# Kernel optimization log

Hardware: AMD Instinct MI355X
Metric: run time of the kernel (lower is better)

## Reference

```python
import jax, jax.numpy as jnp
import numpy as np

ERR = 1e-12


def setup_inputs() -> dict:
    key = jax.random.key(0)
    k1, k2, k3 = jax.random.split(key, 3)
    B, H, L, D = 2, 16, 2048, 64
    k = jax.random.normal(k1, (B, H, L, D), dtype=jnp.float32)
    src = jax.random.uniform(k2, (B, H, L), dtype=jnp.float32)
    dest = jax.random.uniform(k3, (B, H, L), dtype=jnp.float32)
    return {"k": k, "src": src, "dest": dest}


def reference(k, src, dest):
    # k: [B,H,L,D], src/dest: [B,H,L]
    L = k.shape[-2]
    s = jnp.sqrt(src + ERR)   # sqrt-scaled source weights
    d = jnp.sqrt(dest + ERR)  # sqrt-scaled destination weights
    # affinity_1[b,h,i,j] = s_i * d_j * (k_i . k_j), fused as (k*s) @ (k*d)^T
    a1 = jnp.einsum("bhid,bhjd->bhij", k * s[..., :, None], k * d[..., :, None])
    # relu then (x+err)^(2/3)  (kernel: exp2(log2(relu(a)+err) * 2/3))
    a3 = jnp.exp2(jnp.log2(jax.nn.relu(a1) + ERR) * (2.0 / 3.0))
    # forward cumulative sum over j, output causally masked to j >= i
    cs = jnp.cumsum(a3, axis=-1)
    idx = jnp.arange(L)
    mask = idx[:, None] <= idx[None, :]  # keep j >= i
    return jnp.where(mask, cs, 0.0)
```

## Files before the change

### kernel.cpp

```cpp
#include <hip/hip_runtime.h>

#define BH   32
#define LSEQ 2048
#define DDIM 64
#define ERRC 1e-12f

typedef __attribute__((ext_vector_type(8)))  short bf16x8;
typedef __attribute__((ext_vector_type(4)))  float floatx4;
typedef __attribute__((ext_vector_type(4)))  unsigned short ushort4v;

__device__ __forceinline__ unsigned short f2bf(float f) {
    unsigned u = __float_as_uint(f);
    u = u + 0x7FFFu + ((u >> 16) & 1u);
    return (unsigned short)(u >> 16);
}

__device__ __forceinline__ bf16x8 pack8s(const float* __restrict__ p, float w) {
    const floatx4* pv = (const floatx4*)p;
    floatx4 x = pv[0], y = pv[1];
    bf16x8 r;
    r[0] = (short)f2bf(x[0] * w); r[1] = (short)f2bf(x[1] * w);
    r[2] = (short)f2bf(x[2] * w); r[3] = (short)f2bf(x[3] * w);
    r[4] = (short)f2bf(y[0] * w); r[5] = (short)f2bf(y[1] * w);
    r[6] = (short)f2bf(y[2] * w); r[7] = (short)f2bf(y[3] * w);
    return r;
}

__global__ __launch_bounds__(256) void prep_kd(const float* __restrict__ k,
                                               const float* __restrict__ dest,
                                               unsigned short* __restrict__ kd) {
    int idx4 = blockIdx.x * 256 + threadIdx.x;
    int row  = idx4 >> 4;
    float d = sqrtf(dest[row] + ERRC);
    floatx4 v = ((const floatx4*)k)[idx4];
    ushort4v od;
#pragma unroll
    for (int r = 0; r < 4; ++r) od[r] = f2bf(v[r] * d);
    ((ushort4v*)kd)[idx4] = od;
}

__device__ __forceinline__ void load_frag(const unsigned short* __restrict__ p,
                                          bf16x8& lo, bf16x8& hi) {
    lo = *(const bf16x8*)p;
    hi = *(const bf16x8*)(p + 32);
}

__device__ __forceinline__ void load_b_raw(const float* __restrict__ k,
                                           const float* __restrict__ src,
                                           int bhL, int row, int q,
                                           bf16x8& lo, bf16x8& hi) {
    const float* p = k + (long)(bhL + row) * DDIM + q * 8;
    float s = sqrtf(src[bhL + row] + ERRC);
    lo = pack8s(p, s);
    hi = pack8s(p + 32, s);
}

__global__ __launch_bounds__(256, 4) void strip_sums(const unsigned short* __restrict__ kd,
                                                     const float* __restrict__ k,
                                                     const float* __restrict__ src,
                                                     float* __restrict__ S) {
    const int tid  = threadIdx.x;
    const int wave = tid >> 6;
    const int lane = tid & 63;
    const int q    = lane >> 4;
    const int l16  = lane & 15;
    const int bh   = blockIdx.x & 31;
    const int ib   = blockIdx.x >> 5;
    const int i0   = (ib * 4 + wave) * 16;
    const int bhL  = bh * LSEQ;
    const unsigned short* kdb = kd + (long)bh * LSEQ * DDIM;

    bf16x8 blo, bhi;
    load_b_raw(k, src, bhL, i0 + l16, q, blo, bhi);

    bf16x8 aLo[4], aHi[4];
#pragma unroll
    for (int t = 0; t < 4; ++t)
        load_frag(kdb + (long)(16 * t + l16) * DDIM + q * 8, aLo[t], aHi[t]);

    const float c23 = 2.0f / 3.0f;
    float ssv[3];

    for (int cc = 0; cc < 3; ++cc) {
        float ss = 0.f;
        for (int g = 0; g < 8; ++g) {
            const int jn = (cc * 8 + g < 23) ? (cc * 512 + g * 64 + 64) : 0;
            bf16x8 nLo[4], nHi[4];
#pragma unroll
            for (int t = 0; t < 4; ++t)
                load_frag(kdb + (long)(jn + 16 * t + l16) * DDIM + q * 8, nLo[t], nHi[t]);

            floatx4 acc[4];
#pragma unroll
            for (int t = 0; t < 4; ++t) {
                floatx4 z4 = {0.f, 0.f, 0.f, 0.f};
                z4 = __builtin_amdgcn_mfma_f32_16x16x32_bf16(aLo[t], blo, z4, 0, 0, 0);
                acc[t] = __builtin_amdgcn_mfma_f32_16x16x32_bf16(aHi[t], bhi, z4, 0, 0, 0);
            }

            float s = 0.f;
#pragma unroll
            for (int t = 0; t < 4; ++t)
#pragma unroll
                for (int r = 0; r < 4; ++r) {
                    float v = fmaxf(acc[t][r], 0.f) + ERRC;
                    s += exp2f(c23 * __log2f(v));
                }
            float s1 = s + __shfl_xor(s, 16, 64);
            ss += s1 + __shfl_xor(s1, 32, 64);

#pragma unroll
            for (int t = 0; t < 4; ++t) { aLo[t] = nLo[t]; aHi[t] = nHi[t]; }
        }
        ssv[cc] = ss;
    }

    float sv = (q == 0) ? ssv[0] : (q == 1) ? ssv[1] : ssv[2];
    if (q < 3)
        S[(long)(bhL + i0 + l16) * 4 + q] = sv;
}

__global__ __launch_bounds__(128, 4) void chunk_out2(const unsigned short* __restrict__ kd,
                                                     const float* __restrict__ k,
                                                     const float* __restrict__ src,
                                                     const float* __restrict__ S,
                                                     float* __restrict__ out) {
    const int tid  = threadIdx.x;
    const int wave = tid >> 6;
    const int lane = tid & 63;
    const int q    = lane >> 4;
    const int l16  = lane & 15;
    const int u    = blockIdx.x * 2 + wave;
    const int c    = u & 3;
    const int bh   = (u >> 2) & 31;
    const int it   = u >> 7;
    const int i0   = it << 4;
    const int bhL  = bh * LSEQ;
    const int jb   = c << 9;

    if (jb + 512 <= i0) {
        const floatx4 z = {0.f, 0.f, 0.f, 0.f};
#pragma unroll
        for (int s = 0; s < 16; ++s) {
            float* row = out + (long)(bhL + i0 + s) * LSEQ + jb + 4 * lane;
            *(floatx4*)row = z;
            *(floatx4*)(row + 256) = z;
        }
        return;
    }

    const unsigned short* kdb = kd + (long)bh * LSEQ * DDIM;

    bf16x8 blo, bhi;
    load_b_raw(k, src, bhL, i0 + l16, q, blo, bhi);

    float carry = 0.f;
    const float* Sr = S + (long)(bhL + i0 + l16) * 4;
#pragma unroll
    for (int cc = 0; cc < 3; ++cc)
        if (cc < c) carry += Sr[cc];

    const float c23 = 2.0f / 3.0f;

    bf16x8 aLo[4], aHi[4];
#pragma unroll
    for (int t = 0; t < 4; ++t)
        load_frag(kdb + (long)(jb + 16 * t + l16) * DDIM + q * 8, aLo[t], aHi[t]);

    float* orow = out + (long)(bhL + i0 + l16) * LSEQ + q * 4;

    for (int g = 0; g < 8; ++g) {
        const int j0 = jb + (g << 6);
        const int jn = jb + ((g < 7) ? ((g + 1) << 6) : 0);

        bf16x8 nLo[4], nHi[4];
#pragma unroll
        for (int t = 0; t < 4; ++t)
            load_frag(kdb + (long)(jn + 16 * t + l16) * DDIM + q * 8, nLo[t], nHi[t]);

        floatx4 acc[4];
#pragma unroll
        for (int t = 0; t < 4; ++t) {
            floatx4 z4 = {0.f, 0.f, 0.f, 0.f};
            z4 = __builtin_amdgcn_mfma_f32_16x16x32_bf16(aLo[t], blo, z4, 0, 0, 0);
            acc[t] = __builtin_amdgcn_mfma_f32_16x16x32_bf16(aHi[t], bhi, z4, 0, 0, 0);
        }

        float uu[4][4];
#pragma unroll
        for (int t = 0; t < 4; ++t)
#pragma unroll
            for (int r = 0; r < 4; ++r) {
                float v = fmaxf(acc[t][r], 0.f) + ERRC;
                uu[t][r] = exp2f(c23 * __log2f(v));
            }

        if (j0 + 64 <= i0) {
            float s = 0.f;
#pragma unroll
            for (int t = 0; t < 4; ++t)
                s += (uu[t][0] + uu[t][1]) + (uu[t][2] + uu[t][3]);
            float s1 = s + __shfl_xor(s, 16, 64);
            carry += s1 + __shfl_xor(s1, 32, 64);
            const floatx4 z = {0.f, 0.f, 0.f, 0.f};
#pragma unroll
            for (int t = 0; t < 4; ++t)
                *(floatx4*)(orow + j0 + 16 * t) = z;
        } else {
#pragma unroll
            for (int t = 0; t < 4; ++t) {
                const int jt0 = j0 + 16 * t;
                if (jt0 + 16 <= i0) {
                    float s = (uu[t][0] + uu[t][1]) + (uu[t][2] + uu[t][3]);
                    float s1 = s + __shfl_xor(s, 16, 64);
                    carry += s1 + __shfl_xor(s1, 32, 64);
                    const floatx4 z = {0.f, 0.f, 0.f, 0.f};
                    *(floatx4*)(orow + jt0) = z;
                } else {
                    uu[t][1] += uu[t][0];
                    uu[t][2] += uu[t][1];
                    uu[t][3] += uu[t][2];
                    const float Sg  = uu[t][3];
                    const float x16 = __shfl_xor(Sg, 16, 64);
                    const float s1  = Sg + x16;
                    const float x32 = __shfl_xor(s1, 32, 64);
                    const float E = ((q & 1) ? x16 : 0.f) + ((q & 2) ? x32 : 0.f) + carry;
                    carry += s1 + x32;
                    floatx4 o;
                    if (jt0 == i0) {
#pragma unroll
                        for (int r = 0; r < 4; ++r)
                            o[r] = ((q * 4 + r) >= l16) ? (uu[t][r] + E) : 0.f;
                    } else {
#pragma unroll
                        for (int r = 0; r < 4; ++r)
                            o[r] = uu[t][r] + E;
                    }
                    *(floatx4*)(orow + jt0) = o;
                }
            }
        }

#pragma unroll
        for (int t = 0; t < 4; ++t) { aLo[t] = nLo[t]; aHi[t] = nHi[t]; }
    }
}

__device__ __forceinline__ void load_row16_raw(const float* __restrict__ kp, long base, int row,
                                               int q, const float* __restrict__ w, int bhL,
                                               bf16x8& lo, bf16x8& hi) {
    const float* p = kp + base + (long)row * DDIM + q * 8;
    float s = sqrtf(w[bhL + row] + ERRC);
    lo = pack8s(p, s);
    hi = pack8s(p + 32, s);
}

__global__ __launch_bounds__(256, 4) void mha_raw(const float* __restrict__ kp,
                                                  const float* __restrict__ src,
                                                  const float* __restrict__ dest,
                                                  float* __restrict__ out) {
    const int tid  = threadIdx.x;
    const int wave = tid >> 6;
    const int lane = tid & 63;
    const int q    = lane >> 4;
    const int l16  = lane & 15;
    const int bh = blockIdx.x & 31;
    const int ib = blockIdx.x >> 5;
    const int i0 = (ib * 4 + wave) * 16;
    const int bhL = bh * LSEQ;
    const long base = (long)bh * LSEQ * DDIM;

    bf16x8 blo, bhi;
    load_row16_raw(kp, base, i0 + l16, q, src, bhL, blo, bhi);

    float carry = 0.f;
    const float c23 = 2.0f / 3.0f;

    bf16x8 aLo[4], aHi[4];
#pragma unroll
    for (int t = 0; t < 4; ++t)
        load_row16_raw(kp, base, 16 * t + l16, q, dest, bhL, aLo[t], aHi[t]);

    float* orow = out + (long)(bhL + i0 + l16) * LSEQ + q * 4;

    for (int it = 0; it < 32; ++it) {
        const int j0 = it << 6;
        bf16x8 nLo[4], nHi[4];
        const int jn = (it < 31) ? (j0 + 64) : 0;
#pragma unroll
        for (int t = 0; t < 4; ++t)
            load_row16_raw(kp, base, jn + 16 * t + l16, q, dest, bhL, nLo[t], nHi[t]);

        floatx4 acc[4];
#pragma unroll
        for (int t = 0; t < 4; ++t) {
            floatx4 z4 = {0.f, 0.f, 0.f, 0.f};
            z4 = __builtin_amdgcn_mfma_f32_16x16x32_bf16(aLo[t], blo, z4, 0, 0, 0);
            acc[t] = __builtin_amdgcn_mfma_f32_16x16x32_bf16(aHi[t], bhi, z4, 0, 0, 0);
        }

        float uu[4][4];
#pragma unroll
        for (int t = 0; t < 4; ++t)
#pragma unroll
            for (int r = 0; r < 4; ++r) {
                float v = fmaxf(acc[t][r], 0.f) + ERRC;
                uu[t][r] = exp2f(c23 * __log2f(v));
            }

#pragma unroll
        for (int t = 0; t < 4; ++t) {
            const int jt0 = j0 + 16 * t;
            if (jt0 + 16 <= i0) {
                float s = (uu[t][0] + uu[t][1]) + (uu[t][2] + uu[t][3]);
                float s1 = s + __shfl_xor(s, 16, 64);
                carry += s1 + __shfl_xor(s1, 32, 64);
                const floatx4 z = {0.f, 0.f, 0.f, 0.f};
                *(floatx4*)(orow + jt0) = z;
            } else {
                uu[t][1] += uu[t][0];
                uu[t][2] += uu[t][1];
                uu[t][3] += uu[t][2];
                const float Sg  = uu[t][3];
                const float x16 = __shfl_xor(Sg, 16, 64);
                const float s1  = Sg + x16;
                const float x32 = __shfl_xor(s1, 32, 64);
                const float E = ((q & 1) ? x16 : 0.f) + ((q & 2) ? x32 : 0.f) + carry;
                carry += s1 + x32;
                floatx4 o;
                if (jt0 == i0) {
#pragma unroll
                    for (int r = 0; r < 4; ++r)
                        o[r] = ((q * 4 + r) >= l16) ? (uu[t][r] + E) : 0.f;
                } else {
#pragma unroll
                    for (int r = 0; r < 4; ++r)
                        o[r] = uu[t][r] + E;
                }
                *(floatx4*)(orow + jt0) = o;
            }
        }

#pragma unroll
        for (int t = 0; t < 4; ++t) { aLo[t] = nLo[t]; aHi[t] = nHi[t]; }
    }
}

extern "C" void kernel_launch(void* const* d_in, const int* in_sizes, int n_in,
                              void* d_out, int out_size, void* d_ws, size_t ws_size,
                              hipStream_t stream) {
    const float* k    = (const float*)d_in[0];
    const float* src  = (const float*)d_in[1];
    const float* dest = (const float*)d_in[2];
    float* out = (float*)d_out;

    const size_t kdsz = (size_t)BH * LSEQ * DDIM * sizeof(unsigned short);
    const size_t ssz  = (size_t)BH * LSEQ * 4 * sizeof(float);
    if (ws_size >= kdsz + ssz) {
        unsigned short* kd = (unsigned short*)d_ws;
        float* S = (float*)((char*)d_ws + kdsz);
        prep_kd<<<dim3(4096), dim3(256), 0, stream>>>(k, dest, kd);
        strip_sums<<<dim3(1024), dim3(256), 0, stream>>>(kd, k, src, S);
        chunk_out2<<<dim3(8192), dim3(128), 0, stream>>>(kd, k, src, S, out);
    } else {
        mha_raw<<<dim3(1024), dim3(256), 0, stream>>>(k, src, dest, out);
    }
}
```

Baseline: 706.9 us.

## Split strip sums per chunk, drop register prefetch, remap waves for occupancy

The strip-sum kernel now gives each wave a single 512-column chunk, not all three chunks in sequence, so the grid grows threefold and work spreads across more waves. Both kernels drop the double-buffered next-fragment prefetch, which lowers register pressure. Launch bounds rise to 8 blocks per CU and the wave-to-work mapping becomes bh-fastest with 256-thread blocks. The cost is exposed load latency per tile and extra wave launches.

```diff
diff --git a/kernel.cpp b/kernel.cpp
--- a/kernel.cpp
+++ b/kernel.cpp
@@ -55,72 +55,57 @@
     hi = pack8s(p + 32, s);
 }
 
-__global__ __launch_bounds__(256, 4) void strip_sums(const unsigned short* __restrict__ kd,
-                                                     const float* __restrict__ k,
-                                                     const float* __restrict__ src,
-                                                     float* __restrict__ S) {
+__global__ __launch_bounds__(256, 8) void strip_sums2(const unsigned short* __restrict__ kd,
+                                                      const float* __restrict__ k,
+                                                      const float* __restrict__ src,
+                                                      float* __restrict__ S) {
     const int tid  = threadIdx.x;
     const int wave = tid >> 6;
     const int lane = tid & 63;
     const int q    = lane >> 4;
     const int l16  = lane & 15;
-    const int bh   = blockIdx.x & 31;
-    const int ib   = blockIdx.x >> 5;
-    const int i0   = (ib * 4 + wave) * 16;
+    const int u    = blockIdx.x * 4 + wave;
+    const int bh   = u & 31;
+    const int rest = u >> 5;
+    const int it   = rest & 127;
+    const int cc   = rest >> 7;
+    const int i0   = it << 4;
     const int bhL  = bh * LSEQ;
+    const int jb   = cc << 9;
     const unsigned short* kdb = kd + (long)bh * LSEQ * DDIM;
 
     bf16x8 blo, bhi;
     load_b_raw(k, src, bhL, i0 + l16, q, blo, bhi);
 
-    bf16x8 aLo[4], aHi[4];
-#pragma unroll
-    for (int t = 0; t < 4; ++t)
-        load_frag(kdb + (long)(16 * t + l16) * DDIM + q * 8, aLo[t], aHi[t]);
-
     const float c23 = 2.0f / 3.0f;
-    float ssv[3];
-
-    for (int cc = 0; cc < 3; ++cc) {
-        float ss = 0.f;
-        for (int g = 0; g < 8; ++g) {
-            const int jn = (cc * 8 + g < 23) ? (cc * 512 + g * 64 + 64) : 0;
-            bf16x8 nLo[4], nHi[4];
-#pragma unroll
-            for (int t = 0; t < 4; ++t)
-                load_frag(kdb + (long)(jn + 16 * t + l16) * DDIM + q * 8, nLo[t], nHi[t]);
-
-            floatx4 acc[4];
-#pragma unroll
-            for (int t = 0; t < 4; ++t) {
-                floatx4 z4 = {0.f, 0.f, 0.f, 0.f};
-                z4 = __builtin_amdgcn_mfma_f32_16x16x32_bf16(aLo[t], blo, z4, 0, 0, 0);
-                acc[t] = __builtin_amdgcn_mfma_f32_16x16x32_bf16(aHi[t], bhi, z4, 0, 0, 0);
-            }
-
-            float s = 0.f;
-#pragma unroll
-            for (int t = 0; t < 4; ++t)
-#pragma unroll
-                for (int r = 0; r < 4; ++r) {
-                    float v = fmaxf(acc[t][r], 0.f) + ERRC;
-                    s += exp2f(c23 * __log2f(v));
-                }
-            float s1 = s + __shfl_xor(s, 16, 64);
-            ss += s1 + __shfl_xor(s1, 32, 64);
-
-#pragma unroll
-            for (int t = 0; t < 4; ++t) { aLo[t] = nLo[t]; aHi[t] = nHi[t]; }
-        }
-        ssv[cc] = ss;
-    }
-
-    float sv = (q == 0) ? ssv[0] : (q == 1) ? ssv[1] : ssv[2];
-    if (q < 3)
-        S[(long)(bhL + i0 + l16) * 4 + q] = sv;
-}
-
-__global__ __launch_bounds__(128, 4) void chunk_out2(const unsigned short* __restrict__ kd,
+    float ss = 0.f;
+
+    for (int g = 0; g < 8; ++g) {
+        const int j0 = jb + (g << 6);
+        bf16x8 aLo[4], aHi[4];
+#pragma unroll
+        for (int t = 0; t < 4; ++t)
+            load_frag(kdb + (long)(j0 + 16 * t + l16) * DDIM + q * 8, aLo[t], aHi[t]);
+
+#pragma unroll
+        for (int t = 0; t < 4; ++t) {
+            floatx4 z4 = {0.f, 0.f, 0.f, 0.f};
+            z4 = __builtin_amdgcn_mfma_f32_16x16x32_bf16(aLo[t], blo, z4, 0, 0, 0);
+            floatx4 acc = __builtin_amdgcn_mfma_f32_16x16x32_bf16(aHi[t], bhi, z4, 0, 0, 0);
+#pragma unroll
+            for (int r = 0; r < 4; ++r) {
+                float v = fmaxf(acc[r], 0.f) + ERRC;
+                ss += exp2f(c23 * __log2f(v));
+            }
+        }
+    }
+    float s1 = ss + __shfl_xor(ss, 16, 64);
+    ss = s1 + __shfl_xor(s1, 32, 64);
+    if (q == 0)
+        S[(long)(bhL + i0 + l16) * 4 + cc] = ss;
+}
+
+__global__ __launch_bounds__(256, 8) void chunk_out3(const unsigned short* __restrict__ kd,
                                                      const float* __restrict__ k,
                                                      const float* __restrict__ src,
                                                      const float* __restrict__ S,
@@ -130,10 +115,11 @@
     const int lane = tid & 63;
     const int q    = lane >> 4;
     const int l16  = lane & 15;
-    const int u    = blockIdx.x * 2 + wave;
-    const int c    = u & 3;
-    const int bh   = (u >> 2) & 31;
-    const int it   = u >> 7;
+    const int u    = blockIdx.x * 4 + wave;
+    const int bh   = u & 31;
+    const int rest = u >> 5;
+    const int it   = rest & 127;
+    const int c    = rest >> 7;
     const int i0   = it << 4;
     const int bhL  = bh * LSEQ;
     const int jb   = c << 9;
@@ -161,22 +147,15 @@
         if (cc < c) carry += Sr[cc];
 
     const float c23 = 2.0f / 3.0f;
-
-    bf16x8 aLo[4], aHi[4];
-#pragma unroll
-    for (int t = 0; t < 4; ++t)
-        load_frag(kdb + (long)(jb + 16 * t + l16) * DDIM + q * 8, aLo[t], aHi[t]);
-
     float* orow = out + (long)(bhL + i0 + l16) * LSEQ + q * 4;
 
     for (int g = 0; g < 8; ++g) {
         const int j0 = jb + (g << 6);
-        const int jn = jb + ((g < 7) ? ((g + 1) << 6) : 0);
-
-        bf16x8 nLo[4], nHi[4];
-#pragma unroll
-        for (int t = 0; t < 4; ++t)
-            load_frag(kdb + (long)(jn + 16 * t + l16) * DDIM + q * 8, nLo[t], nHi[t]);
+
+        bf16x8 aLo[4], aHi[4];
+#pragma unroll
+        for (int t = 0; t < 4; ++t)
+            load_frag(kdb + (long)(j0 + 16 * t + l16) * DDIM + q * 8, aLo[t], aHi[t]);
 
         floatx4 acc[4];
 #pragma unroll
@@ -240,9 +219,6 @@
                 }
             }
         }
-
-#pragma unroll
-        for (int t = 0; t < 4; ++t) { aLo[t] = nLo[t]; aHi[t] = nHi[t]; }
     }
 }
 
@@ -360,8 +336,8 @@
         unsigned short* kd = (unsigned short*)d_ws;
         float* S = (float*)((char*)d_ws + kdsz);
         prep_kd<<<dim3(4096), dim3(256), 0, stream>>>(k, dest, kd);
-        strip_sums<<<dim3(1024), dim3(256), 0, stream>>>(kd, k, src, S);
-        chunk_out2<<<dim3(8192), dim3(128), 0, stream>>>(kd, k, src, S, out);
+        strip_sums2<<<dim3(3072), dim3(256), 0, stream>>>(kd, k, src, S);
+        chunk_out3<<<dim3(4096), dim3(256), 0, stream>>>(kd, k, src, S, out);
     } else {
         mha_raw<<<dim3(1024), dim3(256), 0, stream>>>(k, src, dest, out);
     }
```

New measurement: 691.1 us. -2.2%, faster.
